# Optimization experiments

Measured on AMD Instinct MI355X. Metric: run time of the kernel, lower is better.

The kernel has to match this reference:

```python
import jax, jax.numpy as jnp
import numpy as np
import math

NUM_HEADS = 8

def setup_inputs() -> dict:
    key = jax.random.key(0)
    ks = jax.random.split(key, 20)
    N, n, M, E = 4096, 3, 16, 256
    nE = 65536
    s = lambda k, shape: (jax.random.normal(k, shape, jnp.float32) * 0.02)
    return {
        "equ": jax.random.normal(ks[0], (N, n, M), jnp.float32),
        "h": jax.random.normal(ks[1], (N, E), jnp.float32),
        "edge_index": jax.random.randint(ks[2], (2, nE), 0, N),
        "edge_fea": jax.random.normal(ks[3], (nE, 4), jnp.float32),
        "W_equ": s(ks[4], (M, E)),
        "W_gproj": s(ks[5], (E, 32)),
        "W_vg": s(ks[6], (E, E)),
        "W_g1": s(ks[7], (32 * 32, 2 * E)), "b_g1": jnp.zeros((2 * E,), jnp.float32),
        "W_g2": s(ks[8], (2 * E, E)), "b_g2": jnp.zeros((E,), jnp.float32),
        "W_q": s(ks[9], (2 * E, E)), "b_q": jnp.zeros((E,), jnp.float32),
        "W_k": s(ks[10], (2 * E, E)), "b_k": jnp.zeros((E,), jnp.float32),
        "W_v": s(ks[11], (2 * E, E)), "b_v": jnp.zeros((E,), jnp.float32),
        "W_ng": s(ks[12], (E, E)), "b_ng": jnp.zeros((E,), jnp.float32),
        "W_gout": s(ks[13], (E, E)),
        "W_gdec": s(ks[14], (E, M)),
        "W_hdec": s(ks[15], (E, E)), "b_hdec": jnp.zeros((E,), jnp.float32),
    }


def reference(equ, h, edge_index, edge_fea, W_equ, W_gproj, W_vg, W_g1, b_g1,
              W_g2, b_g2, W_q, b_q, W_k, b_k, W_v, b_v, W_ng, b_ng,
              W_gout, W_gdec, W_hdec, b_hdec):
    # edge_index / edge_fea are unused in the original forward (dead args).
    N, n, M = equ.shape
    E = W_equ.shape[1]
    H = NUM_HEADS
    D = E // H
    scaling = D ** -0.5
    sqrtE = math.sqrt(E)

    g_src = (equ @ W_equ) * sqrtE                     # [N, n, E]
    h_src = h * sqrtE                                 # [N, E]

    g2 = g_src @ W_gproj                              # [N, n, 32]
    gram = jnp.einsum('nia,nib->nab', g2, g2)         # [N, 32, 32]
    g2 = gram.reshape(N, 32 * 32)
    g2 = jax.nn.relu(g2 @ W_g1 + b_g1) @ W_g2 + b_g2  # [N, E]

    h2 = jnp.concatenate([g2, h_src], axis=-1)        # [N, 2E]
    q = ((h2 @ W_q + b_q) * scaling).reshape(N, H, D)
    k = (h2 @ W_k + b_k).reshape(N, H, D)
    v = (h2 @ W_v + b_v).reshape(N, H, D)
    vg = (g_src @ W_vg).reshape(N, n, H, D)           # [N, n, H, D]

    attn = jax.nn.softmax(jnp.einsum('nhd,mhd->hnm', q, k), axis=-1)  # [H, N, N]

    out_v = jnp.einsum('hnm,mhd->nhd', attn, v).reshape(N, E)
    h_src1 = out_v @ W_ng + b_ng                      # [N, E]

    # Same attention probs reused for the vector channel (torch does repeat+bmm;
    # we broadcast instead of materializing the repeated [n*H, N, N] tensor).
    out_g = jnp.einsum('hnm,mvhd->nvhd', attn, vg).reshape(N, n, E)
    g_src1 = out_g @ W_gout                           # [N, n, E]

    g_src = g_src + g_src1
    h_src = h_src + h_src1
    equ_out = g_src @ W_gdec                          # [N, n, M]
    h_out = h_src @ W_hdec + b_hdec                   # [N, E]
    return (equ_out, h_out)
```

## Files before the change

kernel.cpp:

```cpp
#include <hip/hip_runtime.h>
#include <hip/hip_bf16.h>

typedef __attribute__((ext_vector_type(8))) short short8;
typedef __attribute__((ext_vector_type(4))) float floatx4;

constexpr int N_ = 4096;
constexpr float SQRT_E = 16.0f;
constexpr float QSCALE = 0.17677669529663687f * 1.4426950408889634f;

__device__ __forceinline__ ushort f2bf(float x) {
  __hip_bfloat16 h = __float2bfloat16(x);
  return *reinterpret_cast<ushort*>(&h);
}
__device__ __forceinline__ float bf2f(ushort b) {
  unsigned int u = ((unsigned int)b) << 16;
  return __uint_as_float(u);
}

__device__ __forceinline__ float dpp_max16(float x) {
  int v = __float_as_int(x);
  int y;
  y = __builtin_amdgcn_update_dpp(v, v, 0x128, 0xf, 0xf, false);
  v = __float_as_int(fmaxf(__int_as_float(v), __int_as_float(y)));
  y = __builtin_amdgcn_update_dpp(v, v, 0x124, 0xf, 0xf, false);
  v = __float_as_int(fmaxf(__int_as_float(v), __int_as_float(y)));
  y = __builtin_amdgcn_update_dpp(v, v, 0x122, 0xf, 0xf, false);
  v = __float_as_int(fmaxf(__int_as_float(v), __int_as_float(y)));
  y = __builtin_amdgcn_update_dpp(v, v, 0x121, 0xf, 0xf, false);
  v = __float_as_int(fmaxf(__int_as_float(v), __int_as_float(y)));
  return __int_as_float(v);
}

__device__ __forceinline__ void do_transpose(
    const float* __restrict__ src, ushort* __restrict__ dsth,
    ushort* __restrict__ dstl, int R, int C, int lb, int cb_shift,
    float* smem, int hasLo)
{
  float (*tile)[33] = (float(*)[33])smem;
  const int r0 = (lb >> cb_shift) * 32;
  const int c0 = (lb & ((1 << cb_shift) - 1)) * 32;
  const int tx = threadIdx.x & 31, ty = threadIdx.x >> 5;
  #pragma unroll
  for (int p = 0; p < 4; ++p) {
    const int lr = p*8 + ty;
    tile[lr][tx] = (r0+lr < R && c0+tx < C) ? src[(size_t)(r0+lr)*C + c0 + tx] : 0.f;
  }
  __syncthreads();
  #pragma unroll
  for (int p = 0; p < 4; ++p) {
    const int dc = p*8 + ty;
    if (c0+dc < C && r0+tx < R) {
      const float v = tile[tx][dc];
      const ushort hi = f2bf(v);
      dsth[(size_t)(c0+dc)*R + r0 + tx] = hi;
      if (hasLo) dstl[(size_t)(c0+dc)*R + r0 + tx] = f2bf(v - bf2f(hi));
    }
  }
}

__global__ __launch_bounds__(256) void k_prep(
    const float* __restrict__ equ, const float* __restrict__ h,
    const float* __restrict__ W_equ, const float* __restrict__ W_gproj,
    const float* __restrict__ W_g1, const float* __restrict__ W_g2,
    const float* __restrict__ W_q, const float* __restrict__ W_k,
    const float* __restrict__ W_v, const float* __restrict__ W_vg,
    const float* __restrict__ W_ng, const float* __restrict__ W_gout,
    const float* __restrict__ W_hdec, const float* __restrict__ W_gdec,
    ushort* __restrict__ Wg1t, ushort* __restrict__ Wg2t,
    ushort* __restrict__ Wth, ushort* __restrict__ Wtl,
    ushort* __restrict__ Wvgt, ushort* __restrict__ Wngt,
    ushort* __restrict__ Wgoutt, ushort* __restrict__ Whdect,
    ushort* __restrict__ Wgdect,
    ushort* __restrict__ h2h, ushort* __restrict__ h2l,
    ushort* __restrict__ vt,
    ushort* __restrict__ g_src_b, ushort* __restrict__ gram_b)
{
  __shared__ __align__(16) float smem[1120];
  const int b = blockIdx.x;
  const int t = threadIdx.x;

  if (b < 512) {
    do_transpose(W_g1, Wg1t, nullptr, 1024, 512, b, 4, smem, 0);
  } else if (b < 640) {
    do_transpose(W_g2, Wg2t, nullptr, 512, 256, b-512, 3, smem, 0);
  } else if (b < 768) {
    do_transpose(W_q, Wth, Wtl, 512, 256, b-640, 3, smem, 1);
  } else if (b < 896) {
    do_transpose(W_k, Wth + 256*512, Wtl + 256*512, 512, 256, b-768, 3, smem, 1);
  } else if (b < 1024) {
    do_transpose(W_v, Wth + 512*512, Wtl + 512*512, 512, 256, b-896, 3, smem, 1);
  } else if (b < 1088) {
    do_transpose(W_vg, Wvgt, nullptr, 256, 256, b-1024, 3, smem, 0);
  } else if (b < 1152) {
    do_transpose(W_ng, Wngt, nullptr, 256, 256, b-1088, 3, smem, 0);
  } else if (b < 1216) {
    do_transpose(W_gout, Wgoutt, nullptr, 256, 256, b-1152, 3, smem, 0);
  } else if (b < 1280) {
    do_transpose(W_hdec, Whdect, nullptr, 256, 256, b-1216, 3, smem, 0);
  } else if (b < 1288) {
    do_transpose(W_gdec, Wgdect, nullptr, 256, 16, b-1280, 0, smem, 0);
  } else if (b < 5384) {
    const int i = b - 1288;
    const float v = h[(size_t)i*256 + t] * SQRT_E;
    const ushort hi = f2bf(v);
    h2h[(size_t)i*512 + 256 + t] = hi;
    h2l[(size_t)i*512 + 256 + t] = f2bf(v - bf2f(hi));
  } else if (b < 7432) {
    const int idx = (b - 5384)*256 + t;
    const int n = idx & 4095;
    const int c16 = (idx >> 12) & 15;
    const int hh = idx >> 16;
    vt[((size_t)hh*144 + 128 + c16)*N_ + n] = (c16 == 0) ? (ushort)0x3F80 : (ushort)0;
  } else {
    float* eq   = smem;
    float* gs   = smem + 48;
    float* g2p  = smem + 816;
    float* part = smem + 912;
    const int i = b - 7432;
    if (t < 48) eq[t] = equ[(size_t)i*48 + t];
    __syncthreads();
    #pragma unroll
    for (int j = 0; j < 3; ++j) {
      float s = 0.f;
      #pragma unroll
      for (int m = 0; m < 16; ++m) s += eq[j*16+m] * W_equ[m*256 + t];
      s *= SQRT_E;
      gs[j*256 + t] = s;
      g_src_b[((size_t)i*3 + j)*256 + t] = f2bf(s);
    }
    __syncthreads();
    if (t < 192) {
      const int o = t % 96, half = t / 96;
      const int j = o >> 5, a = o & 31;
      const int e0 = half * 128;
      float s = 0.f;
      for (int e = 0; e < 128; ++e)
        s += gs[j*256 + e0 + e] * W_gproj[(size_t)(e0+e)*32 + a];
      part[t] = s;
    }
    __syncthreads();
    if (t < 96) g2p[t] = part[t] + part[96 + t];
    __syncthreads();
    #pragma unroll
    for (int r = 0; r < 4; ++r) {
      const int idx = r*256 + t;
      const int a = idx >> 5, bb = idx & 31;
      const float s = g2p[a]*g2p[bb] + g2p[32+a]*g2p[32+bb] + g2p[64+a]*g2p[64+bb];
      gram_b[(size_t)i*1024 + idx] = f2bf(s);
    }
  }
}

template<int KTOT>
__device__ __forceinline__ void gemm_core(
    const ushort* __restrict__ A, const ushort* __restrict__ Bt,
    int bM, int bN, floatx4 acc[4], ushort* As, ushort* Bs)
{
  const int t = threadIdx.x;
  const int wave = t >> 6, lane = t & 63, quad = lane >> 4, m = lane & 15;
  #pragma unroll
  for (int ct = 0; ct < 4; ++ct) acc[ct] = {0.f, 0.f, 0.f, 0.f};
  const int ca = t*2, cb = t*2 + 1;
  const int ra = ca >> 3, pa = ca & 7;
  const int rb = cb >> 3, pb = cb & 7;
  const ushort* pA0 = A  + (size_t)(bM+ra)*KTOT + pa*8;
  const ushort* pA1 = A  + (size_t)(bM+rb)*KTOT + pb*8;
  const ushort* pB0 = Bt + (size_t)(bN+ra)*KTOT + pa*8;
  const ushort* pB1 = Bt + (size_t)(bN+rb)*KTOT + pb*8;
  short8 rA0 = *(const short8*)pA0, rA1 = *(const short8*)pA1;
  short8 rB0 = *(const short8*)pB0, rB1 = *(const short8*)pB1;
  for (int k0 = 0; k0 < KTOT; k0 += 64) {
    __syncthreads();
    *(short8*)&As[ra*72 + pa*8] = rA0;
    *(short8*)&As[rb*72 + pb*8] = rA1;
    *(short8*)&Bs[ra*72 + pa*8] = rB0;
    *(short8*)&Bs[rb*72 + pb*8] = rB1;
    if (k0 + 64 < KTOT) {
      pA0 += 64; pA1 += 64; pB0 += 64; pB1 += 64;
      rA0 = *(const short8*)pA0; rA1 = *(const short8*)pA1;
      rB0 = *(const short8*)pB0; rB1 = *(const short8*)pB1;
    }
    __syncthreads();
    #pragma unroll
    for (int ks = 0; ks < 2; ++ks) {
      const short8 af = *(const short8*)&As[(wave*16 + m)*72 + ks*32 + quad*8];
      #pragma unroll
      for (int ct = 0; ct < 4; ++ct) {
        const short8 bf = *(const short8*)&Bs[(ct*16 + m)*72 + ks*32 + quad*8];
        acc[ct] = __builtin_amdgcn_mfma_f32_16x16x32_bf16(af, bf, acc[ct], 0, 0, 0);
      }
    }
  }
}

template<int KTOT>
__device__ __forceinline__ void gemm_core3(
    const ushort* __restrict__ Ah, const ushort* __restrict__ Al,
    const ushort* __restrict__ Bth, const ushort* __restrict__ Btl,
    int bM, int bN, floatx4 acc[4],
    ushort* Ash, ushort* Asl, ushort* Bsh, ushort* Bsl)
{
  const int t = threadIdx.x;
  const int wave = t >> 6, lane = t & 63, quad = lane >> 4, m = lane & 15;
  #pragma unroll
  for (int ct = 0; ct < 4; ++ct) acc[ct] = {0.f, 0.f, 0.f, 0.f};
  const int ca = t*2, cb = t*2 + 1;
  const int ra = ca >> 3, pa = ca & 7;
  const int rb = cb >> 3, pb = cb & 7;
  const ushort* pAh0 = Ah  + (size_t)(bM+ra)*KTOT + pa*8;
  const ushort* pAh1 = Ah  + (size_t)(bM+rb)*KTOT + pb*8;
  const ushort* pAl0 = Al  + (size_t)(bM+ra)*KTOT + pa*8;
  const ushort* pAl1 = Al  + (size_t)(bM+rb)*KTOT + pb*8;
  const ushort* pBh0 = Bth + (size_t)(bN+ra)*KTOT + pa*8;
  const ushort* pBh1 = Bth + (size_t)(bN+rb)*KTOT + pb*8;
  const ushort* pBl0 = Btl + (size_t)(bN+ra)*KTOT + pa*8;
  const ushort* pBl1 = Btl + (size_t)(bN+rb)*KTOT + pb*8;
  short8 rAh0 = *(const short8*)pAh0, rAh1 = *(const short8*)pAh1;
  short8 rAl0 = *(const short8*)pAl0, rAl1 = *(const short8*)pAl1;
  short8 rBh0 = *(const short8*)pBh0, rBh1 = *(const short8*)pBh1;
  short8 rBl0 = *(const short8*)pBl0, rBl1 = *(const short8*)pBl1;
  for (int k0 = 0; k0 < KTOT; k0 += 64) {
    __syncthreads();
    *(short8*)&Ash[ra*72 + pa*8] = rAh0;
    *(short8*)&Ash[rb*72 + pb*8] = rAh1;
    *(short8*)&Asl[ra*72 + pa*8] = rAl0;
    *(short8*)&Asl[rb*72 + pb*8] = rAl1;
    *(short8*)&Bsh[ra*72 + pa*8] = rBh0;
    *(short8*)&Bsh[rb*72 + pb*8] = rBh1;
    *(short8*)&Bsl[ra*72 + pa*8] = rBl0;
    *(short8*)&Bsl[rb*72 + pb*8] = rBl1;
    if (k0 + 64 < KTOT) {
      pAh0 += 64; pAh1 += 64; pAl0 += 64; pAl1 += 64;
      pBh0 += 64; pBh1 += 64; pBl0 += 64; pBl1 += 64;
      rAh0 = *(const short8*)pAh0; rAh1 = *(const short8*)pAh1;
      rAl0 = *(const short8*)pAl0; rAl1 = *(const short8*)pAl1;
      rBh0 = *(const short8*)pBh0; rBh1 = *(const short8*)pBh1;
      rBl0 = *(const short8*)pBl0; rBl1 = *(const short8*)pBl1;
    }
    __syncthreads();
    #pragma unroll
    for (int ks = 0; ks < 2; ++ks) {
      const short8 ah = *(const short8*)&Ash[(wave*16 + m)*72 + ks*32 + quad*8];
      const short8 al = *(const short8*)&Asl[(wave*16 + m)*72 + ks*32 + quad*8];
      #pragma unroll
      for (int ct = 0; ct < 4; ++ct) {
        const short8 bh = *(const short8*)&Bsh[(ct*16 + m)*72 + ks*32 + quad*8];
        const short8 bl = *(const short8*)&Bsl[(ct*16 + m)*72 + ks*32 + quad*8];
        acc[ct] = __builtin_amdgcn_mfma_f32_16x16x32_bf16(ah, bl, acc[ct], 0, 0, 0);
        acc[ct] = __builtin_amdgcn_mfma_f32_16x16x32_bf16(al, bh, acc[ct], 0, 0, 0);
        acc[ct] = __builtin_amdgcn_mfma_f32_16x16x32_bf16(ah, bh, acc[ct], 0, 0, 0);
      }
    }
  }
}

__global__ __launch_bounds__(256) void k_g1(
    const ushort* __restrict__ gram_b, const ushort* __restrict__ Wg1t,
    const float* __restrict__ b_g1, ushort* __restrict__ hidden)
{
  __shared__ __align__(16) ushort As[64*72], Bs[64*72];
  floatx4 acc[4];
  const int bM = blockIdx.x*64, bN = blockIdx.y*64;
  gemm_core<1024>(gram_b, Wg1t, bM, bN, acc, As, Bs);
  const int lane = threadIdx.x & 63, wave = threadIdx.x >> 6;
  const int quad = lane >> 4, m = lane & 15;
  #pragma unroll
  for (int ct = 0; ct < 4; ++ct) {
    const int c = bN + ct*16 + m;
    #pragma unroll
    for (int r = 0; r < 4; ++r) {
      const int i = bM + wave*16 + quad*4 + r;
      hidden[(size_t)i*512 + c] = f2bf(fmaxf(acc[ct][r] + b_g1[c], 0.f));
    }
  }
}

__global__ __launch_bounds__(256) void k_g2(
    const ushort* __restrict__ hidden, const ushort* __restrict__ Wg2t,
    const float* __restrict__ b_g2, ushort* __restrict__ h2h, ushort* __restrict__ h2l)
{
  __shared__ __align__(16) ushort As[64*72], Bs[64*72];
  floatx4 acc[4];
  const int bM = blockIdx.x*64, bN = blockIdx.y*64;
  gemm_core<512>(hidden, Wg2t, bM, bN, acc, As, Bs);
  const int lane = threadIdx.x & 63, wave = threadIdx.x >> 6;
  const int quad = lane >> 4, m = lane & 15;
  #pragma unroll
  for (int ct = 0; ct < 4; ++ct) {
    const int c = bN + ct*16 + m;
    #pragma unroll
    for (int r = 0; r < 4; ++r) {
      const int i = bM + wave*16 + quad*4 + r;
      const float s = acc[ct][r] + b_g2[c];
      const ushort hi = f2bf(s);
      h2h[(size_t)i*512 + c] = hi;
      h2l[(size_t)i*512 + c] = f2bf(s - bf2f(hi));
    }
  }
}

__global__ __launch_bounds__(256) void k_g34(
    const ushort* __restrict__ h2h, const ushort* __restrict__ h2l,
    const ushort* __restrict__ Wth, const ushort* __restrict__ Wtl,
    const float* __restrict__ b_q, const float* __restrict__ b_k,
    const float* __restrict__ b_v,
    const ushort* __restrict__ g_src_b, const ushort* __restrict__ Wvgt,
    float* __restrict__ q_ws, ushort* __restrict__ kh,
    ushort* __restrict__ vt)
{
  __shared__ __align__(16) ushort S0[64*72], S1[64*72], S2[64*72], S3[64*72];
  const int lb = blockIdx.y*192 + blockIdx.x;
  const int lane = threadIdx.x & 63, wave = threadIdx.x >> 6;
  const int quad = lane >> 4, m = lane & 15;
  floatx4 acc[4];
  if (lb < 768) {
    const int bM = (lb & 63)*64, bN = (lb >> 6)*64;
    if (bN < 512) {
      gemm_core3<512>(h2h, h2l, Wth, Wtl, bM, bN, acc, S0, S1, S2, S3);
      #pragma unroll
      for (int ct = 0; ct < 4; ++ct) {
        const int c = bN + ct*16 + m;
        #pragma unroll
        for (int r = 0; r < 4; ++r) {
          const int i = bM + wave*16 + quad*4 + r;
          if (c < 256) {
            const float s = acc[ct][r] + b_q[c];
            q_ws[((size_t)(c >> 5)*N_ + i)*32 + (c & 31)] = s * QSCALE;
          } else {
            const int cc = c - 256;
            const float s = acc[ct][r] + b_k[cc];
            kh[((size_t)(cc >> 5)*N_ + i)*32 + (cc & 31)] = f2bf(s);
          }
        }
      }
    } else {
      gemm_core<512>(h2h, Wth, bM, bN, acc, S0, S1);
      #pragma unroll
      for (int ct = 0; ct < 4; ++ct) {
        const int cc = bN + ct*16 + m - 512;
        #pragma unroll
        for (int r = 0; r < 4; ++r) {
          const int i = bM + wave*16 + quad*4 + r;
          const float s = acc[ct][r] + b_v[cc];
          vt[((size_t)(cc >> 5)*144 + (cc & 31))*N_ + i] = f2bf(s);
        }
      }
    }
  } else {
    const int lb2 = lb - 768;
    const int bM = (lb2 >> 2)*64, bN = (lb2 & 3)*64;
    gemm_core<256>(g_src_b, Wvgt, bM, bN, acc, S0, S1);
    #pragma unroll
    for (int ct = 0; ct < 4; ++ct) {
      const int c = bN + ct*16 + m;
      const int hh = c >> 5, d = c & 31;
      #pragma unroll
      for (int r = 0; r < 4; ++r) {
        const int i3 = bM + wave*16 + quad*4 + r;
        const int i = i3 / 3, j = i3 - 3*i;
        vt[((size_t)hh*144 + 32 + j*32 + d)*N_ + i] = f2bf(acc[ct][r]);
      }
    }
  }
}

__global__ __launch_bounds__(256, 4) void k3_attn(
    const float* __restrict__ q_ws, const ushort* __restrict__ kh,
    const ushort* __restrict__ vt,
    ushort* __restrict__ Po0, ushort* __restrict__ Po1, ushort* __restrict__ Po2,
    float* __restrict__ Pml)
{
  __shared__ __align__(16) ushort Khs[64*40];
  __shared__ __align__(16) ushort Vs[144*64];
  __shared__ __align__(16) ushort Pl[4*16*72];
  __shared__ float li_s[64];

  const int t    = threadIdx.x;
  const int wave = t >> 6;
  const int lane = t & 63;
  const int quad = lane >> 4;
  const int m    = lane & 15;
  const int h    = blockIdx.y;
  const int s    = blockIdx.z;
  const int n0q  = blockIdx.x * 64;

  const int ktb = (s == 0) ? 0  : (s == 1 ? 22 : 43);
  const int kte = (s == 0) ? 22 : (s == 1 ? 43 : 64);

  union { short8 v; ushort u[8]; } Aqh, Aql;
  {
    const float* qp = q_ws + ((size_t)h*N_ + n0q + wave*16 + m)*32 + quad*8;
    #pragma unroll
    for (int jj = 0; jj < 8; ++jj) {
      const float x = qp[jj];
      const ushort hi = f2bf(x);
      Aqh.u[jj] = hi;
      Aql.u[jj] = f2bf(x - bf2f(hi));
    }
  }

  floatx4 Of[9];
  #pragma unroll
  for (int nt = 0; nt < 9; ++nt) Of[nt] = {0.f, 0.f, 0.f, 0.f};
  float mi[4];
  #pragma unroll
  for (int r = 0; r < 4; ++r) mi[r] = -3.0e38f;

  const int krow = t >> 2, kch = (t & 3) * 8;

  const ushort* pKh = kh + ((size_t)h*N_ + ktb*64 + krow)*32 + kch;
  const ushort* pV[4];
  int wV[4];
  #pragma unroll
  for (int p = 0; p < 4; ++p) {
    const int idx = p*256 + t, row = idx >> 3, g = idx & 7;
    pV[p] = vt + ((size_t)h*144 + row)*N_ + ktb*64 + g*8;
    wV[p] = (row*8 + (g ^ (row & 7)))*8;
  }
  const ushort* pV4 = nullptr;
  int wV4 = 0;
  if (t < 128) {
    const int idx = 1024 + t, row = idx >> 3, g = idx & 7;
    pV4 = vt + ((size_t)h*144 + row)*N_ + ktb*64 + g*8;
    wV4 = (row*8 + (g ^ (row & 7)))*8;
  }

  short8 rK0 = *(const short8*)pKh;
  short8 rV[4], rV4e;
  #pragma unroll
  for (int p = 0; p < 4; ++p) rV[p] = *(const short8*)pV[p];
  if (t < 128) rV4e = *(const short8*)pV4;

  for (int kt = ktb; kt < kte; ++kt) {
    __syncthreads();
    *(short8*)&Khs[krow*40 + kch] = rK0;
    #pragma unroll
    for (int p = 0; p < 4; ++p) *(short8*)&Vs[wV[p]] = rV[p];
    if (t < 128) *(short8*)&Vs[wV4] = rV4e;
    if (kt + 1 < kte) {
      pKh += 2048;
      rK0 = *(const short8*)pKh;
      #pragma unroll
      for (int p = 0; p < 4; ++p) { pV[p] += 64; rV[p] = *(const short8*)pV[p]; }
      if (t < 128) { pV4 += 64; rV4e = *(const short8*)pV4; }
    }
    __syncthreads();

    floatx4 sf[4];
    #pragma unroll
    for (int kb = 0; kb < 4; ++kb) {
      const short8 bkh = *(const short8*)&Khs[(kb*16 + m)*40 + quad*8];
      floatx4 sv = {0.f, 0.f, 0.f, 0.f};
      sv = __builtin_amdgcn_mfma_f32_16x16x32_bf16(Aql.v, bkh, sv, 0, 0, 0);
      sv = __builtin_amdgcn_mfma_f32_16x16x32_bf16(Aqh.v, bkh, sv, 0, 0, 0);
      sf[kb] = sv;
    }

    float tm[4];
    bool need = false;
    #pragma unroll
    for (int r = 0; r < 4; ++r) {
      float nm = fmaxf(fmaxf(sf[0][r], sf[1][r]), fmaxf(sf[2][r], sf[3][r]));
      tm[r] = dpp_max16(nm);
      need |= (tm[r] > mi[r] + 20.f);
    }
    if (__any(need)) {
      #pragma unroll
      for (int r = 0; r < 4; ++r) {
        const float mn = fmaxf(mi[r], tm[r]);
        const float al = exp2f(mi[r] - mn);
        mi[r] = mn;
        #pragma unroll
        for (int nt = 0; nt < 9; ++nt) Of[nt][r] *= al;
      }
    }
    float base[4];
    #pragma unroll
    for (int r = 0; r < 4; ++r) base[r] = 1064866805.0f - mi[r]*8388608.0f;
    #pragma unroll
    for (int kb = 0; kb < 4; ++kb)
      #pragma unroll
      for (int r = 0; r < 4; ++r) {
        int pi = (int)(sf[kb][r]*8388608.0f + base[r]);
        pi = pi < 0 ? 0 : pi;
        Pl[wave*1152 + (quad*4 + r)*72 + kb*16 + m] = (ushort)(pi >> 16);
      }

    #pragma unroll
    for (int ks = 0; ks < 2; ++ks) {
      const short8 ap = *(const short8*)&Pl[wave*1152 + m*72 + ks*32 + quad*8];
      #pragma unroll
      for (int nt = 0; nt < 9; ++nt) {
        const int row = nt*16 + m;
        const int pos = (ks*4 + quad) ^ (row & 7);
        const short8 bv = *(const short8*)&Vs[(row*8 + pos)*8];
        Of[nt] = __builtin_amdgcn_mfma_f32_16x16x32_bf16(ap, bv, Of[nt], 0, 0, 0);
      }
    }
  }

  if (m == 0) {
    #pragma unroll
    for (int r = 0; r < 4; ++r) li_s[wave*16 + quad*4 + r] = Of[8][r];
  }
  __syncthreads();
  const floatx4 liv = *(const floatx4*)&li_s[wave*16 + quad*4];
  float linv[4];
  #pragma unroll
  for (int r = 0; r < 4; ++r) linv[r] = 1.0f / liv[r];

  ushort* Po = (s == 0) ? Po0 : ((s == 1) ? Po1 : Po2);
  #pragma unroll
  for (int nt = 0; nt < 8; ++nt) {
    #pragma unroll
    for (int r = 0; r < 4; ++r) {
      const int n = n0q + wave*16 + quad*4 + r;
      Po[((size_t)h*N_ + n)*128 + nt*16 + m] = f2bf(Of[nt][r] * linv[r]);
    }
  }
  if (m == 0) {
    #pragma unroll
    for (int r = 0; r < 4; ++r) {
      const int n = n0q + wave*16 + quad*4 + r;
      Pml[(((size_t)s*8 + h)*N_ + n)*2 + 0] = mi[r];
      Pml[(((size_t)s*8 + h)*N_ + n)*2 + 1] = Of[8][r];
    }
  }
}

__global__ __launch_bounds__(256) void k_merge(
    const ushort* __restrict__ Po0, const ushort* __restrict__ Po1,
    const ushort* __restrict__ Po2, const float* __restrict__ Pml,
    ushort* __restrict__ out_v_b, ushort* __restrict__ out_g_b)
{
  const int idx = blockIdx.x*256 + threadIdx.x;
  const int c0 = (idx & 15) * 8;
  const int n  = (idx >> 4) & 4095;
  const int h  = idx >> 16;
  const float m1 = Pml[(((size_t)0*8 + h)*N_ + n)*2 + 0];
  const float l1 = Pml[(((size_t)0*8 + h)*N_ + n)*2 + 1];
  const float m2 = Pml[(((size_t)1*8 + h)*N_ + n)*2 + 0];
  const float l2 = Pml[(((size_t)1*8 + h)*N_ + n)*2 + 1];
  const float m3 = Pml[(((size_t)2*8 + h)*N_ + n)*2 + 0];
  const float l3 = Pml[(((size_t)2*8 + h)*N_ + n)*2 + 1];
  const float M = fmaxf(fmaxf(m1, m2), m3);
  const float w1 = exp2f(m1 - M) * l1;
  const float w2 = exp2f(m2 - M) * l2;
  const float w3 = exp2f(m3 - M) * l3;
  const float inv = 1.0f / (w1 + w2 + w3);
  union { short8 v; ushort u[8]; } a, b, c, res;
  a.v = *(const short8*)&Po0[((size_t)h*N_ + n)*128 + c0];
  b.v = *(const short8*)&Po1[((size_t)h*N_ + n)*128 + c0];
  c.v = *(const short8*)&Po2[((size_t)h*N_ + n)*128 + c0];
  #pragma unroll
  for (int j = 0; j < 8; ++j)
    res.u[j] = f2bf((w1*bf2f(a.u[j]) + w2*bf2f(b.u[j]) + w3*bf2f(c.u[j])) * inv);
  if (c0 < 32) {
    *(short8*)&out_v_b[(size_t)n*256 + h*32 + c0] = res.v;
  } else {
    const int j = (c0 - 32) >> 5, cc = (c0 - 32) & 31;
    *(short8*)&out_g_b[((size_t)n*3 + j)*256 + h*32 + cc] = res.v;
  }
}

__global__ __launch_bounds__(256) void k56ab(
    const ushort* __restrict__ out_v_b, const ushort* __restrict__ Wngt,
    const float* __restrict__ b_ng, const float* __restrict__ h,
    ushort* __restrict__ tmp_b,
    const ushort* __restrict__ out_g_b, const ushort* __restrict__ Wgoutt,
    const ushort* __restrict__ g_src_b, ushort* __restrict__ gsum_b)
{
  __shared__ __align__(16) ushort As[64*72], Bs[64*72];
  floatx4 acc[4];
  const int lane = threadIdx.x & 63, wave = threadIdx.x >> 6;
  const int quad = lane >> 4, m = lane & 15;
  const int bN = blockIdx.y*64;
  if (blockIdx.x < 64) {
    const int bM = blockIdx.x*64;
    gemm_core<256>(out_v_b, Wngt, bM, bN, acc, As, Bs);
    #pragma unroll
    for (int ct = 0; ct < 4; ++ct) {
      const int c = bN + ct*16 + m;
      #pragma unroll
      for (int r = 0; r < 4; ++r) {
        const int i = bM + wave*16 + quad*4 + r;
        tmp_b[(size_t)i*256 + c] =
            f2bf(acc[ct][r] + b_ng[c] + h[(size_t)i*256 + c] * SQRT_E);
      }
    }
  } else {
    const int bM = (blockIdx.x - 64)*64;
    gemm_core<256>(out_g_b, Wgoutt, bM, bN, acc, As, Bs);
    #pragma unroll
    for (int ct = 0; ct < 4; ++ct) {
      const int c = bN + ct*16 + m;
      #pragma unroll
      for (int r = 0; r < 4; ++r) {
        const int i = bM + wave*16 + quad*4 + r;
        gsum_b[(size_t)i*256 + c] =
            f2bf(acc[ct][r] + bf2f(g_src_b[(size_t)i*256 + c]));
      }
    }
  }
}

__global__ __launch_bounds__(256) void k56cd(
    const ushort* __restrict__ tmp_b, const ushort* __restrict__ Whdect,
    const float* __restrict__ b_hdec,
    const ushort* __restrict__ gsum_b, const ushort* __restrict__ Wgdect,
    float* __restrict__ out)
{
  __shared__ __align__(16) ushort As[64*72], Bs[64*72];
  const int t = threadIdx.x;
  const int lane = t & 63, wave = t >> 6;
  const int quad = lane >> 4, m = lane & 15;
  if (blockIdx.x < 64) {
    floatx4 acc[4];
    const int bM = blockIdx.x*64, bN = blockIdx.y*64;
    gemm_core<256>(tmp_b, Whdect, bM, bN, acc, As, Bs);
    #pragma unroll
    for (int ct = 0; ct < 4; ++ct) {
      const int c = bN + ct*16 + m;
      #pragma unroll
      for (int r = 0; r < 4; ++r) {
        const int i = bM + wave*16 + quad*4 + r;
        out[196608 + (size_t)i*256 + c] = acc[ct][r] + b_hdec[c];
      }
    }
  } else if (blockIdx.y == 0) {
    const int bM = (blockIdx.x - 64)*64;
    floatx4 acc = {0.f, 0.f, 0.f, 0.f};
    const int row = t >> 2, kq = (t & 3) * 8;
    for (int k0 = 0; k0 < 256; k0 += 32) {
      __syncthreads();
      *(short8*)&As[row*40 + kq] = *(const short8*)&gsum_b[(size_t)(bM+row)*256 + k0 + kq];
      if (t < 64)
        *(short8*)&Bs[(t>>2)*40 + kq] = *(const short8*)&Wgdect[(size_t)(t>>2)*256 + k0 + kq];
      __syncthreads();
      const short8 af = *(const short8*)&As[(wave*16 + m)*40 + quad*8];
      const short8 bf = *(const short8*)&Bs[m*40 + quad*8];
      acc = __builtin_amdgcn_mfma_f32_16x16x32_bf16(af, bf, acc, 0, 0, 0);
    }
    #pragma unroll
    for (int r = 0; r < 4; ++r)
      out[(size_t)(bM + wave*16 + quad*4 + r)*16 + m] = acc[r];
  }
}

extern "C" void kernel_launch(void* const* d_in, const int* in_sizes, int n_in,
                              void* d_out, int out_size, void* d_ws, size_t ws_size,
                              hipStream_t stream) {
  const float* equ    = (const float*)d_in[0];
  const float* h      = (const float*)d_in[1];
  const float* W_equ  = (const float*)d_in[4];
  const float* W_gproj= (const float*)d_in[5];
  const float* W_vg   = (const float*)d_in[6];
  const float* W_g1   = (const float*)d_in[7];
  const float* b_g1   = (const float*)d_in[8];
  const float* W_g2   = (const float*)d_in[9];
  const float* b_g2   = (const float*)d_in[10];
  const float* W_q    = (const float*)d_in[11];
  const float* b_q    = (const float*)d_in[12];
  const float* W_k    = (const float*)d_in[13];
  const float* b_k    = (const float*)d_in[14];
  const float* W_v    = (const float*)d_in[15];
  const float* b_v    = (const float*)d_in[16];
  const float* W_ng   = (const float*)d_in[17];
  const float* b_ng   = (const float*)d_in[18];
  const float* W_gout = (const float*)d_in[19];
  const float* W_gdec = (const float*)d_in[20];
  const float* W_hdec = (const float*)d_in[21];
  const float* b_hdec = (const float*)d_in[22];
  float* out = (float*)d_out;

  char* wsb = (char*)d_ws;
  constexpr size_t MiB = 1048576;
  float*  q_ws    = (float*) (wsb +  0*MiB);
  ushort* kh      = (ushort*)(wsb +  4*MiB);
  ushort* vt      = (ushort*)(wsb +  8*MiB);
  ushort* h2h     = (ushort*)(wsb + 17*MiB);
  ushort* h2l     = (ushort*)(wsb + 21*MiB);
  ushort* g_src_b = (ushort*)(wsb + 25*MiB);
  ushort* wbase   = (ushort*)(wsb + 31*MiB);
  ushort* Wg1t = wbase;
  ushort* Wg2t = wbase + 524288;
  ushort* Wth  = wbase + 655360;
  ushort* Wtl  = wbase + 1048576;
  ushort* Wvgt = wbase + 1441792;
  ushort* wbase2  = (ushort*)(wsb + 34*MiB);
  ushort* Wngt   = wbase2;
  ushort* Wgoutt = wbase2 + 65536;
  ushort* Whdect = wbase2 + 131072;
  ushort* Wgdect = wbase2 + 196608;
  ushort* gram_b  = (ushort*)(wsb + 34*MiB + 524288);
  ushort* hidden  = (ushort*)(wsb + 42*MiB + 524288);
  ushort* Po0     = (ushort*)(wsb + 17*MiB);
  ushort* Po1     = (ushort*)(wsb + 34*MiB + 524288);
  ushort* Po2     = (ushort*)(wsb + 42*MiB + 524288);
  float*  Pml     = (float*) (wsb + 50*MiB + 524288);
  ushort* out_v_b = (ushort*)(wsb +  4*MiB);
  ushort* out_g_b = (ushort*)(wsb +  8*MiB);
  ushort* tmp_b   = (ushort*)(wsb + 42*MiB + 524288);
  ushort* gsum_b  = (ushort*)(wsb + 34*MiB + 524288);

  k_prep<<<11528, 256, 0, stream>>>(
      equ, h, W_equ, W_gproj, W_g1, W_g2, W_q, W_k, W_v,
      W_vg, W_ng, W_gout, W_hdec, W_gdec,
      Wg1t, Wg2t, Wth, Wtl, Wvgt, Wngt, Wgoutt, Whdect, Wgdect,
      h2h, h2l, vt, g_src_b, gram_b);

  k_g1<<<dim3(64, 8), 256, 0, stream>>>(gram_b, Wg1t, b_g1, hidden);
  k_g2<<<dim3(64, 4), 256, 0, stream>>>(hidden, Wg2t, b_g2, h2h, h2l);
  k_g34<<<dim3(192, 8), 256, 0, stream>>>(h2h, h2l, Wth, Wtl, b_q, b_k, b_v,
                                          g_src_b, Wvgt, q_ws, kh, vt);

  dim3 g3(64, 8, 3);
  k3_attn<<<g3, 256, 0, stream>>>(q_ws, kh, vt, Po0, Po1, Po2, Pml);
  k_merge<<<2048, 256, 0, stream>>>(Po0, Po1, Po2, Pml, out_v_b, out_g_b);

  k56ab<<<dim3(256, 4), 256, 0, stream>>>(out_v_b, Wngt, b_ng, h, tmp_b,
                                          out_g_b, Wgoutt, g_src_b, gsum_b);
  k56cd<<<dim3(256, 4), 256, 0, stream>>>(tmp_b, Whdect, b_hdec,
                                          gsum_b, Wgdect, out);
}
```

Before: 272.8 us.

## Split attention keys into four chunks and precompute g_src@W_gdec in prep

Result: slower. 280.2 us (+2.7%).

```diff
diff --git a/kernel.cpp b/kernel.cpp
--- a/kernel.cpp
+++ b/kernel.cpp
@@ -73,7 +73,8 @@
     ushort* __restrict__ Wgdect,
     ushort* __restrict__ h2h, ushort* __restrict__ h2l,
     ushort* __restrict__ vt,
-    ushort* __restrict__ g_src_b, ushort* __restrict__ gram_b)
+    ushort* __restrict__ g_src_b, ushort* __restrict__ gram_b,
+    float* __restrict__ pre0)
 {
   __shared__ __align__(16) float smem[1120];
   const int b = blockIdx.x;
@@ -148,6 +149,21 @@
       const float s = g2p[a]*g2p[bb] + g2p[32+a]*g2p[32+bb] + g2p[64+a]*g2p[64+bb];
       gram_b[(size_t)i*1024 + idx] = f2bf(s);
     }
+    if (t < 192) {
+      const int j = t >> 6, ks = (t >> 4) & 3, mc = t & 15;
+      const int e0 = ks * 64;
+      float s = 0.f;
+      for (int e = 0; e < 64; ++e)
+        s += gs[j*256 + e0 + e] * W_gdec[(size_t)(e0 + e)*16 + mc];
+      part[t] = s;
+    }
+    __syncthreads();
+    if (t < 48) {
+      const int j = t >> 4, mc = t & 15;
+      pre0[((size_t)i*3 + j)*16 + mc] =
+          part[j*64 + mc] + part[j*64 + 16 + mc] +
+          part[j*64 + 32 + mc] + part[j*64 + 48 + mc];
+    }
   }
 }
 
@@ -367,7 +383,8 @@
 __global__ __launch_bounds__(256, 4) void k3_attn(
     const float* __restrict__ q_ws, const ushort* __restrict__ kh,
     const ushort* __restrict__ vt,
-    ushort* __restrict__ Po0, ushort* __restrict__ Po1, ushort* __restrict__ Po2,
+    ushort* __restrict__ Po0, ushort* __restrict__ Po1,
+    ushort* __restrict__ Po2, ushort* __restrict__ Po3,
     float* __restrict__ Pml)
 {
   __shared__ __align__(16) ushort Khs[64*40];
@@ -384,8 +401,8 @@
   const int s    = blockIdx.z;
   const int n0q  = blockIdx.x * 64;
 
-  const int ktb = (s == 0) ? 0  : (s == 1 ? 22 : 43);
-  const int kte = (s == 0) ? 22 : (s == 1 ? 43 : 64);
+  const int ktb = s * 16;
+  const int kte = ktb + 16;
 
   union { short8 v; ushort u[8]; } Aqh, Aql;
   {
@@ -509,7 +526,7 @@
   #pragma unroll
   for (int r = 0; r < 4; ++r) linv[r] = 1.0f / liv[r];
 
-  ushort* Po = (s == 0) ? Po0 : ((s == 1) ? Po1 : Po2);
+  ushort* Po = (s == 0) ? Po0 : ((s == 1) ? Po1 : ((s == 2) ? Po2 : Po3));
   #pragma unroll
   for (int nt = 0; nt < 8; ++nt) {
     #pragma unroll
@@ -530,31 +547,34 @@
 
 __global__ __launch_bounds__(256) void k_merge(
     const ushort* __restrict__ Po0, const ushort* __restrict__ Po1,
-    const ushort* __restrict__ Po2, const float* __restrict__ Pml,
+    const ushort* __restrict__ Po2, const ushort* __restrict__ Po3,
+    const float* __restrict__ Pml,
     ushort* __restrict__ out_v_b, ushort* __restrict__ out_g_b)
 {
   const int idx = blockIdx.x*256 + threadIdx.x;
   const int c0 = (idx & 15) * 8;
   const int n  = (idx >> 4) & 4095;
   const int h  = idx >> 16;
-  const float m1 = Pml[(((size_t)0*8 + h)*N_ + n)*2 + 0];
-  const float l1 = Pml[(((size_t)0*8 + h)*N_ + n)*2 + 1];
-  const float m2 = Pml[(((size_t)1*8 + h)*N_ + n)*2 + 0];
-  const float l2 = Pml[(((size_t)1*8 + h)*N_ + n)*2 + 1];
-  const float m3 = Pml[(((size_t)2*8 + h)*N_ + n)*2 + 0];
-  const float l3 = Pml[(((size_t)2*8 + h)*N_ + n)*2 + 1];
-  const float M = fmaxf(fmaxf(m1, m2), m3);
-  const float w1 = exp2f(m1 - M) * l1;
-  const float w2 = exp2f(m2 - M) * l2;
-  const float w3 = exp2f(m3 - M) * l3;
-  const float inv = 1.0f / (w1 + w2 + w3);
-  union { short8 v; ushort u[8]; } a, b, c, res;
+  float mm[4], ll[4];
+  #pragma unroll
+  for (int s = 0; s < 4; ++s) {
+    mm[s] = Pml[(((size_t)s*8 + h)*N_ + n)*2 + 0];
+    ll[s] = Pml[(((size_t)s*8 + h)*N_ + n)*2 + 1];
+  }
+  const float M = fmaxf(fmaxf(mm[0], mm[1]), fmaxf(mm[2], mm[3]));
+  float w[4], tot = 0.f;
+  #pragma unroll
+  for (int s = 0; s < 4; ++s) { w[s] = exp2f(mm[s] - M) * ll[s]; tot += w[s]; }
+  const float inv = 1.0f / tot;
+  union { short8 v; ushort u[8]; } a, b, c, d, res;
   a.v = *(const short8*)&Po0[((size_t)h*N_ + n)*128 + c0];
   b.v = *(const short8*)&Po1[((size_t)h*N_ + n)*128 + c0];
   c.v = *(const short8*)&Po2[((size_t)h*N_ + n)*128 + c0];
+  d.v = *(const short8*)&Po3[((size_t)h*N_ + n)*128 + c0];
   #pragma unroll
   for (int j = 0; j < 8; ++j)
-    res.u[j] = f2bf((w1*bf2f(a.u[j]) + w2*bf2f(b.u[j]) + w3*bf2f(c.u[j])) * inv);
+    res.u[j] = f2bf((w[0]*bf2f(a.u[j]) + w[1]*bf2f(b.u[j]) +
+                     w[2]*bf2f(c.u[j]) + w[3]*bf2f(d.u[j])) * inv);
   if (c0 < 32) {
     *(short8*)&out_v_b[(size_t)n*256 + h*32 + c0] = res.v;
   } else {
@@ -568,7 +588,7 @@
     const float* __restrict__ b_ng, const float* __restrict__ h,
     ushort* __restrict__ tmp_b,
     const ushort* __restrict__ out_g_b, const ushort* __restrict__ Wgoutt,
-    const ushort* __restrict__ g_src_b, ushort* __restrict__ gsum_b)
+    ushort* __restrict__ gsum_b)
 {
   __shared__ __align__(16) ushort As[64*72], Bs[64*72];
   floatx4 acc[4];
@@ -597,8 +617,7 @@
       #pragma unroll
       for (int r = 0; r < 4; ++r) {
         const int i = bM + wave*16 + quad*4 + r;
-        gsum_b[(size_t)i*256 + c] =
-            f2bf(acc[ct][r] + bf2f(g_src_b[(size_t)i*256 + c]));
+        gsum_b[(size_t)i*256 + c] = f2bf(acc[ct][r]);
       }
     }
   }
@@ -608,6 +627,7 @@
     const ushort* __restrict__ tmp_b, const ushort* __restrict__ Whdect,
     const float* __restrict__ b_hdec,
     const ushort* __restrict__ gsum_b, const ushort* __restrict__ Wgdect,
+    const float* __restrict__ pre0,
     float* __restrict__ out)
 {
   __shared__ __align__(16) ushort As[64*72], Bs[64*72];
@@ -642,8 +662,10 @@
       acc = __builtin_amdgcn_mfma_f32_16x16x32_bf16(af, bf, acc, 0, 0, 0);
     }
     #pragma unroll
-    for (int r = 0; r < 4; ++r)
-      out[(size_t)(bM + wave*16 + quad*4 + r)*16 + m] = acc[r];
+    for (int r = 0; r < 4; ++r) {
+      const int i3 = bM + wave*16 + quad*4 + r;
+      out[(size_t)i3*16 + m] = acc[r] + pre0[(size_t)i3*16 + m];
+    }
   }
 }
 
@@ -677,6 +699,8 @@
   constexpr size_t MiB = 1048576;
   float*  q_ws    = (float*) (wsb +  0*MiB);
   ushort* kh      = (ushort*)(wsb +  4*MiB);
+  float*  Pml     = (float*) (wsb +  6*MiB);
+  float*  pre0    = (float*) (wsb +  7*MiB);
   ushort* vt      = (ushort*)(wsb +  8*MiB);
   ushort* h2h     = (ushort*)(wsb + 17*MiB);
   ushort* h2l     = (ushort*)(wsb + 21*MiB);
@@ -687,39 +711,39 @@
   ushort* Wth  = wbase + 655360;
   ushort* Wtl  = wbase + 1048576;
   ushort* Wvgt = wbase + 1441792;
-  ushort* wbase2  = (ushort*)(wsb + 34*MiB);
+  ushort* gram_b  = (ushort*)(wsb + 34*MiB);
+  ushort* hidden  = (ushort*)(wsb + 42*MiB);
+  ushort* Po0     = (ushort*)(wsb + 17*MiB);
+  ushort* Po1     = (ushort*)(wsb + 25*MiB);
+  ushort* Po2     = (ushort*)(wsb + 34*MiB);
+  ushort* Po3     = (ushort*)(wsb + 42*MiB);
+  ushort* wbase2  = (ushort*)(wsb + 50*MiB);
   ushort* Wngt   = wbase2;
   ushort* Wgoutt = wbase2 + 65536;
   ushort* Whdect = wbase2 + 131072;
   ushort* Wgdect = wbase2 + 196608;
-  ushort* gram_b  = (ushort*)(wsb + 34*MiB + 524288);
-  ushort* hidden  = (ushort*)(wsb + 42*MiB + 524288);
-  ushort* Po0     = (ushort*)(wsb + 17*MiB);
-  ushort* Po1     = (ushort*)(wsb + 34*MiB + 524288);
-  ushort* Po2     = (ushort*)(wsb + 42*MiB + 524288);
-  float*  Pml     = (float*) (wsb + 50*MiB + 524288);
   ushort* out_v_b = (ushort*)(wsb +  4*MiB);
   ushort* out_g_b = (ushort*)(wsb +  8*MiB);
-  ushort* tmp_b   = (ushort*)(wsb + 42*MiB + 524288);
-  ushort* gsum_b  = (ushort*)(wsb + 34*MiB + 524288);
+  ushort* tmp_b   = (ushort*)(wsb + 17*MiB);
+  ushort* gsum_b  = (ushort*)(wsb + 25*MiB);
 
   k_prep<<<11528, 256, 0, stream>>>(
       equ, h, W_equ, W_gproj, W_g1, W_g2, W_q, W_k, W_v,
       W_vg, W_ng, W_gout, W_hdec, W_gdec,
       Wg1t, Wg2t, Wth, Wtl, Wvgt, Wngt, Wgoutt, Whdect, Wgdect,
-      h2h, h2l, vt, g_src_b, gram_b);
+      h2h, h2l, vt, g_src_b, gram_b, pre0);
 
   k_g1<<<dim3(64, 8), 256, 0, stream>>>(gram_b, Wg1t, b_g1, hidden);
   k_g2<<<dim3(64, 4), 256, 0, stream>>>(hidden, Wg2t, b_g2, h2h, h2l);
   k_g34<<<dim3(192, 8), 256, 0, stream>>>(h2h, h2l, Wth, Wtl, b_q, b_k, b_v,
                                           g_src_b, Wvgt, q_ws, kh, vt);
 
-  dim3 g3(64, 8, 3);
-  k3_attn<<<g3, 256, 0, stream>>>(q_ws, kh, vt, Po0, Po1, Po2, Pml);
-  k_merge<<<2048, 256, 0, stream>>>(Po0, Po1, Po2, Pml, out_v_b, out_g_b);
+  dim3 g3(64, 8, 4);
+  k3_attn<<<g3, 256, 0, stream>>>(q_ws, kh, vt, Po0, Po1, Po2, Po3, Pml);
+  k_merge<<<2048, 256, 0, stream>>>(Po0, Po1, Po2, Po3, Pml, out_v_b, out_g_b);
 
   k56ab<<<dim3(256, 4), 256, 0, stream>>>(out_v_b, Wngt, b_ng, h, tmp_b,
-                                          out_g_b, Wgoutt, g_src_b, gsum_b);
+                                          out_g_b, Wgoutt, gsum_b);
   k56cd<<<dim3(256, 4), 256, 0, stream>>>(tmp_b, Whdect, b_hdec,
-                                          gsum_b, Wgdect, out);
-}
+                                          gsum_b, Wgdect, pre0, out);
+}
```
